# Performance work log

Hardware: AMD Instinct MI355X
Metric: run time of the kernel (lower is better)

Reference implementation:

```python
import jax, jax.numpy as jnp
import numpy as np

TOP_K = 2

def setup_inputs() -> dict:
    key = jax.random.key(0)
    k1, k2 = jax.random.split(key)
    N, D, E = 16384, 2048, 64
    x = jax.random.normal(k1, (N, D), dtype=jnp.float32)
    W = jax.random.normal(k2, (D, E), dtype=jnp.float32) * (1.0 / np.sqrt(D))
    b = jnp.zeros((E,), dtype=jnp.float32)
    return {"x": x, "W": W, "b": b}

def reference(x, W, b):
    # gate linear: [N, D] @ [D, E] + [E]
    logits = jnp.einsum('nd,de->ne', x, W) + b
    gates = jax.nn.softmax(logits, axis=-1)
    topk_vals, topk_idx = jax.lax.top_k(gates, TOP_K)  # [N, k]
    N = gates.shape[0]
    rows = jnp.arange(N)[:, None]  # [N, 1] broadcast over k
    dispatch_mask = jnp.zeros_like(gates).at[rows, topk_idx].set(topk_vals)
    return dispatch_mask, topk_idx
```

## Files before the change

### kernel.cpp

```cpp
#include <hip/hip_runtime.h>
#include <math.h>

#define NROWS 16384
#define DDIM  2048
#define EEXP  64
#define RB    32
#define KC    64
#define NCH   (DDIM / KC)

#define WSPLIT_BYTES 786432
#define CHSTRIDE     24576

typedef short  bf16x8 __attribute__((ext_vector_type(8)));
typedef float  f32x16 __attribute__((ext_vector_type(16)));

union V4 { uint4 u; bf16x8 s; };

static __device__ __forceinline__ void split3x2(float f0, float f1,
                                                unsigned int &p0, unsigned int &p1,
                                                unsigned int &p2) {
    unsigned int a0 = __float_as_uint(f0), b0 = __float_as_uint(f1);
    unsigned int ah = a0 & 0xffff0000u,   bh = b0 & 0xffff0000u;
    float fa1 = f0 - __uint_as_float(ah);
    float fb1 = f1 - __uint_as_float(bh);
    unsigned int a1 = __float_as_uint(fa1), b1 = __float_as_uint(fb1);
    unsigned int am = a1 & 0xffff0000u,     bm = b1 & 0xffff0000u;
    float fa2 = fa1 - __uint_as_float(am);
    float fb2 = fb1 - __uint_as_float(bm);
    p0 = (a0 >> 16) | bh;
    p1 = (a1 >> 16) | bm;
    p2 = (__float_as_uint(fa2) >> 16) | (__float_as_uint(fb2) & 0xffff0000u);
}

static __device__ __forceinline__ void cvt8(float4 u, float4 v, V4 &q0, V4 &q1, V4 &q2) {
    split3x2(u.x, u.y, q0.u.x, q1.u.x, q2.u.x);
    split3x2(u.z, u.w, q0.u.y, q1.u.y, q2.u.y);
    split3x2(v.x, v.y, q0.u.z, q1.u.z, q2.u.z);
    split3x2(v.z, v.w, q0.u.w, q1.u.w, q2.u.w);
}

#define MM(ACC, A, B) ACC = __builtin_amdgcn_mfma_f32_32x32x16_bf16((A), (B), ACC, 0, 0, 0)

#define MM6(A0, A1, A2, B0, B1, B2)                                \
    MM(accA, (A0).s, (B0).s); MM(accB, (A0).s, (B1).s);            \
    MM(accA, (A1).s, (B0).s); MM(accB, (A0).s, (B2).s);            \
    MM(accA, (A1).s, (B1).s); MM(accB, (A2).s, (B0).s);

__global__ __launch_bounds__(256)
void wsplit_kernel(const float* __restrict__ W, unsigned char* __restrict__ ws) {
    const int t  = blockIdx.x * 256 + threadIdx.x;
    const int e  = t & 63;
    const int ko = t >> 6;
    const int k0 = ko * 8;
    float f[8];
#pragma unroll
    for (int j = 0; j < 8; ++j) f[j] = W[(size_t)(k0 + j) * EEXP + e];
    V4 q0, q1, q2;
    cvt8(make_float4(f[0], f[1], f[2], f[3]),
         make_float4(f[4], f[5], f[6], f[7]), q0, q1, q2);
    const int c  = k0 >> 6;
    const int kg = (k0 >> 4) & 3;
    const int h  = (k0 >> 3) & 1;
    const int et = e >> 5;
    const int ln = h * 32 + (e & 31);
    unsigned char* d = ws + (size_t)(((((c * 4 + kg) * 2 + et) * 64) + ln) * 48);
    *(uint4*)(d +  0) = q0.u;
    *(uint4*)(d + 16) = q1.u;
    *(uint4*)(d + 32) = q2.u;
}

__global__ __launch_bounds__(512, 4)
void router_kernel(const float* __restrict__ x,
                   const unsigned char* __restrict__ wsplit,
                   const float* __restrict__ bias_v,
                   float* __restrict__ mask_out,
                   float* __restrict__ idx_out) {
    __shared__ __align__(16) float ep[8192];

    const int tid  = threadIdx.x;
    const int lane = tid & 63;
    const int w    = __builtin_amdgcn_readfirstlane(tid >> 6);
    const int kg   = w & 3;
    const int et   = w >> 2;
    const int row0 = blockIdx.x * RB;
    const int l31  = lane & 31;
    const int h    = lane >> 5;

    const float* xp = x + (size_t)(row0 + l31) * DDIM + kg * 16 + h * 8;
    const unsigned char* wp = wsplit + (size_t)(((kg * 2 + et) * 64 + lane) * 48);

    f32x16 accA, accB;
#pragma unroll
    for (int i = 0; i < 16; ++i) { accA[i] = 0.f; accB[i] = 0.f; }

    float4 x0a = *(const float4*)(xp);
    float4 x0b = *(const float4*)(xp + 4);
    V4 b00, b01, b02, b10, b11, b12;
    b00.u = *(const uint4*)(wp);
    b01.u = *(const uint4*)(wp + 16);
    b02.u = *(const uint4*)(wp + 32);
    float4 x1a = *(const float4*)(xp + KC);
    float4 x1b = *(const float4*)(xp + KC + 4);
    b10.u = *(const uint4*)(wp + CHSTRIDE);
    b11.u = *(const uint4*)(wp + CHSTRIDE + 16);
    b12.u = *(const uint4*)(wp + CHSTRIDE + 32);

#pragma unroll 1
    for (int c = 0; c < NCH; c += 2) {
        V4 a0, a1, a2;
        cvt8(x0a, x0b, a0, a1, a2);
        if (c + 2 < NCH) {
            x0a = *(const float4*)(xp + (c + 2) * KC);
            x0b = *(const float4*)(xp + (c + 2) * KC + 4);
        }
        MM6(a0, a1, a2, b00, b01, b02)
        if (c + 2 < NCH) {
            const unsigned char* q = wp + (size_t)(c + 2) * CHSTRIDE;
            b00.u = *(const uint4*)(q);
            b01.u = *(const uint4*)(q + 16);
            b02.u = *(const uint4*)(q + 32);
        }
        cvt8(x1a, x1b, a0, a1, a2);
        if (c + 3 < NCH) {
            x1a = *(const float4*)(xp + (c + 3) * KC);
            x1b = *(const float4*)(xp + (c + 3) * KC + 4);
        }
        MM6(a0, a1, a2, b10, b11, b12)
        if (c + 3 < NCH) {
            const unsigned char* q = wp + (size_t)(c + 3) * CHSTRIDE;
            b10.u = *(const uint4*)(q);
            b11.u = *(const uint4*)(q + 16);
            b12.u = *(const uint4*)(q + 32);
        }
    }

#pragma unroll
    for (int r = 0; r < 16; ++r) {
        const int rowl = (r & 3) + 8 * (r >> 2) + 4 * h;
        ep[kg * 2048 + rowl * 64 + et * 32 + l31] = accA[r] + accB[r];
    }
    __syncthreads();

    const float bias = bias_v[lane];
#pragma unroll
    for (int rr = 0; rr < 4; ++rr) {
        const int rl  = w * 4 + rr;
        const int row = row0 + rl;
        float logit = bias + ep[rl * 64 + lane]
                           + ep[2048 + rl * 64 + lane]
                           + ep[4096 + rl * 64 + lane]
                           + ep[6144 + rl * 64 + lane];

        float m = logit;
#pragma unroll
        for (int off = 32; off >= 1; off >>= 1) m = fmaxf(m, __shfl_xor(m, off));
        float ex = __expf(logit - m);
        float s = ex;
#pragma unroll
        for (int off = 32; off >= 1; off >>= 1) s += __shfl_xor(s, off);
        float gate = ex / s;

        float v1 = logit; int i1 = lane;
#pragma unroll
        for (int off = 32; off >= 1; off >>= 1) {
            float ov = __shfl_xor(v1, off);
            int   oi = __shfl_xor(i1, off);
            if (ov > v1 || (ov == v1 && oi < i1)) { v1 = ov; i1 = oi; }
        }
        float v2 = (lane == i1) ? -INFINITY : logit; int i2 = lane;
#pragma unroll
        for (int off = 32; off >= 1; off >>= 1) {
            float ov = __shfl_xor(v2, off);
            int   oi = __shfl_xor(i2, off);
            if (ov > v2 || (ov == v2 && oi < i2)) { v2 = ov; i2 = oi; }
        }

        float outv = (lane == i1 || lane == i2) ? gate : 0.0f;
        mask_out[(size_t)row * EEXP + lane] = outv;
        if (lane == 0) {
            idx_out[row * 2 + 0] = (float)i1;
            idx_out[row * 2 + 1] = (float)i2;
        }
    }
}

extern "C" void kernel_launch(void* const* d_in, const int* in_sizes, int n_in,
                              void* d_out, int out_size, void* d_ws, size_t ws_size,
                              hipStream_t stream) {
    const float* x = (const float*)d_in[0];
    const float* W = (const float*)d_in[1];
    const float* b = (const float*)d_in[2];
    float* mask_out = (float*)d_out;
    float* idx_out  = mask_out + (size_t)NROWS * EEXP;
    unsigned char* ws = (unsigned char*)d_ws;

    wsplit_kernel<<<dim3(64), dim3(256), 0, stream>>>(W, ws);
    router_kernel<<<dim3(NROWS / RB), dim3(512), 0, stream>>>(x, ws, b, mask_out, idx_out);
}
```

Baseline: 238.2 us.

## Deepen global-load prefetch to eight chunks with inline-asm loads and explicit vmcnt waits

Replaces the two-chunk register double buffer in the router GEMM loop with an eight-stage software pipeline. Each stage holds one chunk of x and the split W in registers, issued through inline global_load_dwordx4 with immediate offsets, and each stage waits on an explicit s_waitcnt vmcnt. Occupancy in launch_bounds drops from 4 to 2 to make room for the much larger register footprint. The aim is to keep more memory requests in flight per wave and hide HBM latency, at the cost of fewer resident waves and hand-managed wait counts that must match the number of loads issued.

```diff
diff --git a/kernel.cpp b/kernel.cpp
--- a/kernel.cpp
+++ b/kernel.cpp
@@ -11,10 +11,12 @@
 #define WSPLIT_BYTES 786432
 #define CHSTRIDE     24576
 
-typedef short  bf16x8 __attribute__((ext_vector_type(8)));
-typedef float  f32x16 __attribute__((ext_vector_type(16)));
-
-union V4 { uint4 u; bf16x8 s; };
+typedef short        bf16x8 __attribute__((ext_vector_type(8)));
+typedef float        f32x16 __attribute__((ext_vector_type(16)));
+typedef float        f32x4  __attribute__((ext_vector_type(4)));
+typedef unsigned int u32x4  __attribute__((ext_vector_type(4)));
+
+union V4 { u32x4 u; bf16x8 s; };
 
 static __device__ __forceinline__ void split3x2(float f0, float f1,
                                                 unsigned int &p0, unsigned int &p1,
@@ -32,19 +34,39 @@
     p2 = (__float_as_uint(fa2) >> 16) | (__float_as_uint(fb2) & 0xffff0000u);
 }
 
-static __device__ __forceinline__ void cvt8(float4 u, float4 v, V4 &q0, V4 &q1, V4 &q2) {
-    split3x2(u.x, u.y, q0.u.x, q1.u.x, q2.u.x);
-    split3x2(u.z, u.w, q0.u.y, q1.u.y, q2.u.y);
-    split3x2(v.x, v.y, q0.u.z, q1.u.z, q2.u.z);
-    split3x2(v.z, v.w, q0.u.w, q1.u.w, q2.u.w);
+static __device__ __forceinline__ void cvt8(f32x4 u, f32x4 v, V4 &q0, V4 &q1, V4 &q2) {
+    unsigned int a, b, c;
+    split3x2(u[0], u[1], a, b, c); q0.u[0] = a; q1.u[0] = b; q2.u[0] = c;
+    split3x2(u[2], u[3], a, b, c); q0.u[1] = a; q1.u[1] = b; q2.u[1] = c;
+    split3x2(v[0], v[1], a, b, c); q0.u[2] = a; q1.u[2] = b; q2.u[2] = c;
+    split3x2(v[2], v[3], a, b, c); q0.u[3] = a; q1.u[3] = b; q2.u[3] = c;
 }
 
 #define MM(ACC, A, B) ACC = __builtin_amdgcn_mfma_f32_32x32x16_bf16((A), (B), ACC, 0, 0, 0)
 
-#define MM6(A0, A1, A2, B0, B1, B2)                                \
-    MM(accA, (A0).s, (B0).s); MM(accB, (A0).s, (B1).s);            \
-    MM(accA, (A1).s, (B0).s); MM(accB, (A0).s, (B2).s);            \
-    MM(accA, (A1).s, (B1).s); MM(accB, (A2).s, (B0).s);
+#define STR_(x) #x
+#define GLD(dst, voff, base, IMM)                                             \
+    asm volatile("global_load_dwordx4 %0, %1, %2 offset:" STR_(IMM)           \
+                 : "=v"(dst) : "v"(voff), "s"(base))
+#define WAITV(N)                                                              \
+    asm volatile("s_waitcnt vmcnt(" STR_(N) ")" ::: "memory");                \
+    __builtin_amdgcn_sched_barrier(0)
+
+#define CONSUME(XA, XB, B0, B1, B2) {                                         \
+    V4 a0, a1, a2; cvt8(XA, XB, a0, a1, a2);                                  \
+    MM(accA, a0.s, B0.s); MM(accB, a0.s, B1.s); MM(accA, a1.s, B0.s);         \
+    MM(accB, a0.s, B2.s); MM(accA, a1.s, B1.s); MM(accB, a2.s, B0.s); }
+
+#define ISSUE(XA, XB, B0, B1, B2, IMM0, IMM1)                                 \
+    GLD(XA, voffx, x, IMM0); GLD(XB, voffx, x, IMM1);                         \
+    GLD(B0.u, voffB, wsplit, 0); GLD(B1.u, voffB, wsplit, 16);                \
+    GLD(B2.u, voffB, wsplit, 32); voffB += CHSTRIDE;
+
+#define STEP(N, XA, XB, B0, B1, B2, IMM0, IMM1)                               \
+    WAITV(N); CONSUME(XA, XB, B0, B1, B2) ISSUE(XA, XB, B0, B1, B2, IMM0, IMM1)
+
+#define DRAIN(N, XA, XB, B0, B1, B2)                                          \
+    WAITV(N); CONSUME(XA, XB, B0, B1, B2)
 
 __global__ __launch_bounds__(256)
 void wsplit_kernel(const float* __restrict__ W, unsigned char* __restrict__ ws) {
@@ -52,24 +74,25 @@
     const int e  = t & 63;
     const int ko = t >> 6;
     const int k0 = ko * 8;
-    float f[8];
-#pragma unroll
-    for (int j = 0; j < 8; ++j) f[j] = W[(size_t)(k0 + j) * EEXP + e];
+    f32x4 u, v;
+#pragma unroll
+    for (int j = 0; j < 4; ++j) u[j] = W[(size_t)(k0 + j) * EEXP + e];
+#pragma unroll
+    for (int j = 0; j < 4; ++j) v[j] = W[(size_t)(k0 + 4 + j) * EEXP + e];
     V4 q0, q1, q2;
-    cvt8(make_float4(f[0], f[1], f[2], f[3]),
-         make_float4(f[4], f[5], f[6], f[7]), q0, q1, q2);
+    cvt8(u, v, q0, q1, q2);
     const int c  = k0 >> 6;
     const int kg = (k0 >> 4) & 3;
     const int h  = (k0 >> 3) & 1;
     const int et = e >> 5;
     const int ln = h * 32 + (e & 31);
     unsigned char* d = ws + (size_t)(((((c * 4 + kg) * 2 + et) * 64) + ln) * 48);
-    *(uint4*)(d +  0) = q0.u;
-    *(uint4*)(d + 16) = q1.u;
-    *(uint4*)(d + 32) = q2.u;
-}
-
-__global__ __launch_bounds__(512, 4)
+    *(u32x4*)(d +  0) = q0.u;
+    *(u32x4*)(d + 16) = q1.u;
+    *(u32x4*)(d + 32) = q2.u;
+}
+
+__global__ __launch_bounds__(512, 2)
 void router_kernel(const float* __restrict__ x,
                    const unsigned char* __restrict__ wsplit,
                    const float* __restrict__ bias_v,
@@ -86,53 +109,49 @@
     const int l31  = lane & 31;
     const int h    = lane >> 5;
 
-    const float* xp = x + (size_t)(row0 + l31) * DDIM + kg * 16 + h * 8;
-    const unsigned char* wp = wsplit + (size_t)(((kg * 2 + et) * 64 + lane) * 48);
+    unsigned int voffx = (unsigned int)(((row0 + l31) * DDIM + kg * 16 + h * 8) * 4);
+    unsigned int voffB = (unsigned int)(((kg * 2 + et) * 64 + lane) * 48);
 
     f32x16 accA, accB;
 #pragma unroll
     for (int i = 0; i < 16; ++i) { accA[i] = 0.f; accB[i] = 0.f; }
 
-    float4 x0a = *(const float4*)(xp);
-    float4 x0b = *(const float4*)(xp + 4);
-    V4 b00, b01, b02, b10, b11, b12;
-    b00.u = *(const uint4*)(wp);
-    b01.u = *(const uint4*)(wp + 16);
-    b02.u = *(const uint4*)(wp + 32);
-    float4 x1a = *(const float4*)(xp + KC);
-    float4 x1b = *(const float4*)(xp + KC + 4);
-    b10.u = *(const uint4*)(wp + CHSTRIDE);
-    b11.u = *(const uint4*)(wp + CHSTRIDE + 16);
-    b12.u = *(const uint4*)(wp + CHSTRIDE + 32);
+    f32x4 X0a, X0b, X1a, X1b, X2a, X2b, X3a, X3b;
+    f32x4 X4a, X4b, X5a, X5b, X6a, X6b, X7a, X7b;
+    V4 B00, B01, B02, B10, B11, B12, B20, B21, B22, B30, B31, B32;
+    V4 B40, B41, B42, B50, B51, B52, B60, B61, B62, B70, B71, B72;
+
+    ISSUE(X0a, X0b, B00, B01, B02,    0,   16)
+    ISSUE(X1a, X1b, B10, B11, B12,  256,  272)
+    ISSUE(X2a, X2b, B20, B21, B22,  512,  528)
+    ISSUE(X3a, X3b, B30, B31, B32,  768,  784)
+    ISSUE(X4a, X4b, B40, B41, B42, 1024, 1040)
+    ISSUE(X5a, X5b, B50, B51, B52, 1280, 1296)
+    ISSUE(X6a, X6b, B60, B61, B62, 1536, 1552)
+    ISSUE(X7a, X7b, B70, B71, B72, 1792, 1808)
+    voffx += 2048;
 
 #pragma unroll 1
-    for (int c = 0; c < NCH; c += 2) {
-        V4 a0, a1, a2;
-        cvt8(x0a, x0b, a0, a1, a2);
-        if (c + 2 < NCH) {
-            x0a = *(const float4*)(xp + (c + 2) * KC);
-            x0b = *(const float4*)(xp + (c + 2) * KC + 4);
-        }
-        MM6(a0, a1, a2, b00, b01, b02)
-        if (c + 2 < NCH) {
-            const unsigned char* q = wp + (size_t)(c + 2) * CHSTRIDE;
-            b00.u = *(const uint4*)(q);
-            b01.u = *(const uint4*)(q + 16);
-            b02.u = *(const uint4*)(q + 32);
-        }
-        cvt8(x1a, x1b, a0, a1, a2);
-        if (c + 3 < NCH) {
-            x1a = *(const float4*)(xp + (c + 3) * KC);
-            x1b = *(const float4*)(xp + (c + 3) * KC + 4);
-        }
-        MM6(a0, a1, a2, b10, b11, b12)
-        if (c + 3 < NCH) {
-            const unsigned char* q = wp + (size_t)(c + 3) * CHSTRIDE;
-            b10.u = *(const uint4*)(q);
-            b11.u = *(const uint4*)(q + 16);
-            b12.u = *(const uint4*)(q + 32);
-        }
+    for (int j = 0; j < 3; ++j) {
+        STEP(35, X0a, X0b, B00, B01, B02,    0,   16)
+        STEP(35, X1a, X1b, B10, B11, B12,  256,  272)
+        STEP(35, X2a, X2b, B20, B21, B22,  512,  528)
+        STEP(35, X3a, X3b, B30, B31, B32,  768,  784)
+        STEP(35, X4a, X4b, B40, B41, B42, 1024, 1040)
+        STEP(35, X5a, X5b, B50, B51, B52, 1280, 1296)
+        STEP(35, X6a, X6b, B60, B61, B62, 1536, 1552)
+        STEP(35, X7a, X7b, B70, B71, B72, 1792, 1808)
+        voffx += 2048;
     }
+
+    DRAIN(35, X0a, X0b, B00, B01, B02)
+    DRAIN(30, X1a, X1b, B10, B11, B12)
+    DRAIN(25, X2a, X2b, B20, B21, B22)
+    DRAIN(20, X3a, X3b, B30, B31, B32)
+    DRAIN(15, X4a, X4b, B40, B41, B42)
+    DRAIN(10, X5a, X5b, B50, B51, B52)
+    DRAIN(5,  X6a, X6b, B60, B61, B62)
+    DRAIN(0,  X7a, X7b, B70, B71, B72)
 
 #pragma unroll
     for (int r = 0; r < 16; ++r) {
```

After: 241.7 us. Within noise of the previous version (+1.5%).
